# Kernel optimization log

Hardware: AMD Instinct MI355X
Metric: run time of the kernel (lower is better)

## Reference

```python
import jax, jax.numpy as jnp
import numpy as np

T, B, C, H, W = 128, 16, 4, 84, 84
NUM_ACTIONS, FEAT, HID = 18, 512, 256


def _conv(x, w, b, stride):
    # x: (N,C,H,W), w: (O,I,kh,kw)
    y = jax.lax.conv_general_dilated(
        x, w, window_strides=(stride, stride), padding='VALID',
        dimension_numbers=('NCHW', 'OIHW', 'NCHW'))
    return y + b[None, :, None, None]


def setup_inputs() -> dict:
    key = jax.random.key(0)
    ks = jax.random.split(key, 24)
    s = 0.05
    inp = {
        'obs_seq': jax.random.uniform(ks[0], (T, B, C, H, W), jnp.float32) * 255.0,
        'actions_seq': jax.random.randint(ks[1], (T, B), 0, NUM_ACTIONS),
        'episode_starts_seq': jax.random.randint(ks[2], (T, B), 0, 2).astype(jnp.float32),
        'h0': jnp.zeros((1, B, HID), jnp.float32),
        'c0': jnp.zeros((1, B, HID), jnp.float32),
        # NatureCNN params
        'conv1_w': jax.random.normal(ks[3], (32, C, 8, 8)) * s,
        'conv1_b': jnp.zeros((32,)),
        'conv2_w': jax.random.normal(ks[4], (64, 32, 4, 4)) * s,
        'conv2_b': jnp.zeros((64,)),
        'conv3_w': jax.random.normal(ks[5], (64, 64, 3, 3)) * s,
        'conv3_b': jnp.zeros((64,)),
        'fc_w': jax.random.normal(ks[6], (FEAT, 64 * 7 * 7)) * s,
        'fc_b': jnp.zeros((FEAT,)),
        # LSTM params (torch gate order i,f,g,o)
        'w_ih': jax.random.normal(ks[7], (4 * HID, FEAT)) * s,
        'w_hh': jax.random.normal(ks[8], (4 * HID, HID)) * s,
        'b_ih': jnp.zeros((4 * HID,)),
        'b_hh': jnp.zeros((4 * HID,)),
        # heads
        'actor_w': jax.random.normal(ks[9], (NUM_ACTIONS, HID)) * 0.01,
        'actor_b': jnp.zeros((NUM_ACTIONS,)),
        'critic_w': jax.random.normal(ks[10], (1, HID)) * s,
        'critic_b': jnp.zeros((1,)),
        'aux_w': jax.random.normal(ks[11], (1, FEAT)) * s,
        'aux_b': jnp.zeros((1,)),
    }
    return inp


def reference(obs_seq, actions_seq, episode_starts_seq, h0, c0,
              conv1_w, conv1_b, conv2_w, conv2_b, conv3_w, conv3_b,
              fc_w, fc_b, w_ih, w_hh, b_ih, b_hh,
              actor_w, actor_b, critic_w, critic_b, aux_w, aux_b):
    t, b = actions_seq.shape
    x = obs_seq.reshape(t * b, *obs_seq.shape[2:]) / 255.0
    x = jax.nn.relu(_conv(x, conv1_w, conv1_b, 4))   # (TB,32,20,20)
    x = jax.nn.relu(_conv(x, conv2_w, conv2_b, 2))   # (TB,64,9,9)
    x = jax.nn.relu(_conv(x, conv3_w, conv3_b, 1))   # (TB,64,7,7)
    feat = jax.nn.relu(x.reshape(t * b, -1) @ fc_w.T + fc_b)  # (TB,FEAT)

    aux_logits = (feat @ aux_w.T + aux_b).squeeze(-1).reshape(t, b)
    feat_seq = feat.reshape(t, b, -1)

    def step(carry, inp):
        h, c = carry
        x_t, s_t = inp
        keep = (1.0 - s_t)[:, None]
        h = h * keep
        c = c * keep
        gates = x_t @ w_ih.T + b_ih + h @ w_hh.T + b_hh  # (B,4H)
        i, f, g, o = jnp.split(gates, 4, axis=-1)
        c = jax.nn.sigmoid(f) * c + jax.nn.sigmoid(i) * jnp.tanh(g)
        h = jax.nn.sigmoid(o) * jnp.tanh(c)
        return (h, c), h

    _, out = jax.lax.scan(step, (h0[0], c0[0]), (feat_seq, episode_starts_seq))  # (T,B,HID)

    logits = out @ actor_w.T + actor_b
    logp = jax.nn.log_softmax(logits, axis=-1)
    log_probs = jnp.take_along_axis(logp, actions_seq[..., None], axis=-1).squeeze(-1)
    entropy = -jnp.sum(jnp.exp(logp) * logp, axis=-1)
    values = (out @ critic_w.T + critic_b).squeeze(-1)
    return log_probs, entropy, values, aux_logits
```

## Files before the change

### kernel.cpp

```cpp
#include <hip/hip_runtime.h>
#include <hip/hip_bf16.h>
#include <cstddef>

typedef __attribute__((ext_vector_type(8))) short bf16x8;
typedef __attribute__((ext_vector_type(8))) unsigned short u16x8;
typedef __attribute__((ext_vector_type(4))) float f32x4;

static constexpr size_t OFF_X1B   = 0;
static constexpr size_t OFF_X2B   = 52428800;
static constexpr size_t OFF_X3B   = 73662464;
static constexpr size_t OFF_FEATB = 86507520;
static constexpr size_t OFF_W2B   = 88604672;
static constexpr size_t OFF_W3B   = 88670208;
static constexpr size_t OFF_FCWB  = 88743936;
static constexpr size_t OFF_WIHB  = 91955200;
static constexpr size_t OFF_GX    = 97198080;
static constexpr size_t OFF_HSEQ  = 105586688;
static constexpr size_t OFF_W1B   = 108732416;
static constexpr size_t OFF_WHHB  = 108748800;
static constexpr size_t OFF_ORDB  = 109273088;
static constexpr size_t OFF_ORDT0 = 109281280;
static constexpr size_t OFF_ORDLEN= 109289472;
static constexpr size_t OFF_NSEG  = 109297664;
static constexpr size_t OFF_FCPART= 109305856;

__device__ __forceinline__ float sigmoidf_(float x) {
  return 1.0f / (1.0f + __expf(-x));
}
__device__ __forceinline__ float tanhf_(float x) {
  return 1.0f - 2.0f / (__expf(2.0f * x) + 1.0f);
}
__device__ __forceinline__ short f2bfs(float x) {
  union { __hip_bfloat16 b; short s; } cv;
  cv.b = __float2bfloat16(x);
  return cv.s;
}

__global__ __launch_bounds__(256) void prep_kernel(
    const float* __restrict__ c1w, const float* __restrict__ c2w,
    const float* __restrict__ c3w, const float* __restrict__ fcw,
    const float* __restrict__ wih, const float* __restrict__ whh,
    __hip_bfloat16* __restrict__ w1b,
    __hip_bfloat16* __restrict__ w2b, __hip_bfloat16* __restrict__ w3b,
    __hip_bfloat16* __restrict__ fcwb, __hip_bfloat16* __restrict__ wihb,
    __hip_bfloat16* __restrict__ whhb) {
  int i = blockIdx.x * 256 + threadIdx.x;
  if (i < 32768) {
    int o = i >> 9, k = i & 511;
    int pos = k >> 5, ci = k & 31;
    int ky = pos >> 2, kx = pos & 3;
    w2b[i] = __float2bfloat16(c2w[o * 512 + ci * 16 + ky * 4 + kx]);
  } else if (i < 69632) {
    int j = i - 32768;
    int o = j / 576, k = j - o * 576;
    int pos = k >> 6, ci = k & 63;
    int ky = pos / 3, kx = pos - ky * 3;
    w3b[j] = __float2bfloat16(c3w[o * 576 + ci * 9 + ky * 3 + kx]);
  } else if (i < 1675264) {
    int j = i - 69632;
    int o = j / 3136, k = j - o * 3136;
    int sp = k >> 6, ci = k & 63;
    fcwb[j] = __float2bfloat16(fcw[o * 3136 + ci * 49 + sp]);
  } else if (i < 2199552) {
    int j = i - 1675264;
    wihb[j] = __float2bfloat16(wih[j]);
  } else if (i < 2461696) {
    int j = i - 2199552;
    whhb[j] = __float2bfloat16(whh[j]);
  } else if (i < 2469888) {
    int j = i - 2461696;
    int oc = j >> 8, k = j & 255;
    int ky = k >> 5, rem = k & 31;
    int ci = rem >> 3, kx = rem & 7;
    w1b[j] = __float2bfloat16(c1w[oc * 256 + ci * 64 + ky * 8 + kx] * (1.0f / 255.0f));
  }
}

__global__ __launch_bounds__(256) void plan_kernel(
    const float* __restrict__ starts, int* __restrict__ ord_b,
    int* __restrict__ ord_t0, int* __restrict__ ord_len,
    int* __restrict__ nseg_out) {
  __shared__ float s_starts[2048];
  __shared__ int s_t0[2048];
  __shared__ int s_len[2048];
  __shared__ int cnt[16];
  __shared__ int hist[132];
  __shared__ int off[132];
  const int tid = threadIdx.x;
  {
    float4* d = (float4*)s_starts;
    const float4* s = (const float4*)starts;
#pragma unroll
    for (int i = 0; i < 2; ++i) d[tid + i * 256] = s[tid + i * 256];
  }
  if (tid < 132) hist[tid] = 0;
  __syncthreads();
  if (tid < 16) {
    int b = tid, c = 0;
    for (int t = 0; t < 128; ++t) {
      float s = s_starts[t * 16 + b];
      if (t == 0 || s != 0.0f) {
        if (c > 0) s_len[b * 128 + c - 1] = t - s_t0[b * 128 + c - 1];
        s_t0[b * 128 + c] = t;
        ++c;
      }
    }
    s_len[b * 128 + c - 1] = 128 - s_t0[b * 128 + c - 1];
    cnt[b] = c;
  }
  __syncthreads();
  for (int idx = tid; idx < 2048; idx += 256) {
    int b = idx >> 7, i = idx & 127;
    if (i < cnt[b]) atomicAdd(&hist[s_len[idx]], 1);
  }
  __syncthreads();
  if (tid == 0) {
    int running = 0;
    for (int L = 128; L >= 1; --L) { off[L] = running; running += hist[L]; }
    *nseg_out = running;
  }
  __syncthreads();
  for (int idx = tid; idx < 2048; idx += 256) {
    int b = idx >> 7, i = idx & 127;
    if (i < cnt[b]) {
      int len = s_len[idx];
      int pos = atomicAdd(&off[len], 1);
      ord_b[pos] = b;
      ord_t0[pos] = s_t0[idx];
      ord_len[pos] = len;
    }
  }
}

__global__ __launch_bounds__(256, 2) void conv1_rs(
    const float* __restrict__ obs, const __hip_bfloat16* __restrict__ w1b,
    const float* __restrict__ b1, __hip_bfloat16* __restrict__ x1b) {
  constexpr int LDW = 264;
  __shared__ __align__(16) __hip_bfloat16 Ws[32 * LDW];
  const int tid = threadIdx.x;
  const int wv = tid >> 6, l = tid & 63;
  const int lane16 = l & 15, quad = l >> 4;
  for (int i = tid; i < 1024; i += 256) {
    const int r = i >> 5, c = (i & 31) * 8;
    *(uint4*)&Ws[r * LDW + c] = *(const uint4*)&w1b[r * 256 + c];
  }
  const int m0 = blockIdx.x * 256 + wv * 64;
  const float* abase[4];
#pragma unroll
  for (int mf = 0; mf < 4; ++mf) {
    const int m = m0 + mf * 16 + lane16;
    const int n = m / 400, sp = m - n * 400;
    const int oy = sp / 20, ox = sp - oy * 20;
    abase[mf] = obs + (size_t)n * 28224 + quad * 7056 + (oy * 4) * 84 + ox * 4;
  }
  f32x4 acc[4][2] = {};
  __syncthreads();
#pragma unroll 2
  for (int s = 0; s < 8; ++s) {
    bf16x8 bfr[2];
#pragma unroll
    for (int nf = 0; nf < 2; ++nf)
      bfr[nf] = *(const bf16x8*)&Ws[(nf * 16 + lane16) * LDW + s * 32 + quad * 8];
#pragma unroll
    for (int mf = 0; mf < 4; ++mf) {
      const float4 p = *(const float4*)(abase[mf] + s * 84);
      const float4 q = *(const float4*)(abase[mf] + s * 84 + 4);
      bf16x8 a;
      a[0] = f2bfs(p.x); a[1] = f2bfs(p.y); a[2] = f2bfs(p.z); a[3] = f2bfs(p.w);
      a[4] = f2bfs(q.x); a[5] = f2bfs(q.y); a[6] = f2bfs(q.z); a[7] = f2bfs(q.w);
      acc[mf][0] = __builtin_amdgcn_mfma_f32_16x16x32_bf16(a, bfr[0], acc[mf][0], 0, 0, 0);
      acc[mf][1] = __builtin_amdgcn_mfma_f32_16x16x32_bf16(a, bfr[1], acc[mf][1], 0, 0, 0);
    }
  }
#pragma unroll
  for (int nf = 0; nf < 2; ++nf) {
    const int col = nf * 16 + lane16;
    const float bb = b1[col];
#pragma unroll
    for (int mf = 0; mf < 4; ++mf)
#pragma unroll
      for (int r = 0; r < 4; ++r) {
        const int row = m0 + mf * 16 + quad * 4 + r;
        x1b[(size_t)row * 32 + col] =
            __float2bfloat16(fmaxf(acc[mf][nf][r] + bb, 0.f));
      }
  }
}

template<int KK, int LDW, int MODE>
__global__ __launch_bounds__(256, 2) void conv_rs(
    const __hip_bfloat16* __restrict__ A, const __hip_bfloat16* __restrict__ Wb,
    const float* __restrict__ bias, __hip_bfloat16* __restrict__ Cb) {
  __shared__ __align__(16) __hip_bfloat16 Ws[64 * LDW];
  const int tid = threadIdx.x;
  const int wv = tid >> 6, l = tid & 63;
  const int lane16 = l & 15, quad = l >> 4;
  constexpr int CPR = KK / 8;
  constexpr int CH = 64 * CPR;
  for (int i = tid; i < CH; i += 256) {
    const int r = i / CPR;
    const int c = (i - r * CPR) * 8;
    *(uint4*)&Ws[r * LDW + c] = *(const uint4*)&Wb[r * KK + c];
  }
  const int m0 = blockIdx.x * 256 + wv * 64;
  const __hip_bfloat16* abase[4];
#pragma unroll
  for (int mf = 0; mf < 4; ++mf) {
    const int m = m0 + mf * 16 + lane16;
    if (MODE == 1) {
      const int n = m / 81, sp = m - n * 81;
      const int oy = sp / 9, ox = sp - oy * 9;
      abase[mf] = A + ((n * 20 + oy * 2) * 20 + ox * 2) * 32 + quad * 8;
    } else {
      const int n = m / 49, sp = m - n * 49;
      const int oy = sp / 7, ox = sp - oy * 7;
      abase[mf] = A + ((n * 9 + oy) * 9 + ox) * 64 + quad * 8;
    }
  }
  f32x4 acc[4][4] = {};
  __syncthreads();
  constexpr int KS = KK / 32;
#pragma unroll
  for (int s = 0; s < KS; ++s) {
    int koff;
    if (MODE == 1) {
      koff = ((s >> 2) * 20 + (s & 3)) * 32;
    } else {
      const int pos = s >> 1;
      koff = ((pos / 3) * 9 + (pos % 3)) * 64 + (s & 1) * 32;
    }
    bf16x8 bfr[4];
#pragma unroll
    for (int nf = 0; nf < 4; ++nf)
      bfr[nf] = *(const bf16x8*)&Ws[(nf * 16 + lane16) * LDW + s * 32 + quad * 8];
#pragma unroll
    for (int mf = 0; mf < 4; ++mf) {
      const bf16x8 a = *(const bf16x8*)(abase[mf] + koff);
#pragma unroll
      for (int nf = 0; nf < 4; ++nf)
        acc[mf][nf] = __builtin_amdgcn_mfma_f32_16x16x32_bf16(a, bfr[nf], acc[mf][nf], 0, 0, 0);
    }
  }
#pragma unroll
  for (int nf = 0; nf < 4; ++nf) {
    const int col = nf * 16 + lane16;
    const float bb = bias[col];
#pragma unroll
    for (int mf = 0; mf < 4; ++mf)
#pragma unroll
      for (int r = 0; r < 4; ++r) {
        const int row = m0 + mf * 16 + quad * 4 + r;
        Cb[(size_t)row * 64 + col] =
            __float2bfloat16(fmaxf(acc[mf][nf][r] + bb, 0.f));
      }
  }
}

template<int BM, int MODE>
__global__ __launch_bounds__(256) void gemm_mfma(
    const __hip_bfloat16* __restrict__ Abase,
    const __hip_bfloat16* __restrict__ Wb,
    const float* __restrict__ bias1, const float* __restrict__ bias2,
    float* __restrict__ Cf, __hip_bfloat16* __restrict__ Cb,
    const int M, const int N, const int K, const int relu,
    float* __restrict__ Cpart) {
  constexpr int LDK = 40;
  __shared__ __align__(16) __hip_bfloat16 As[BM * LDK];
  __shared__ __align__(16) __hip_bfloat16 Ws[64 * LDK];
  const int tid = threadIdx.x;
  const int m0 = blockIdx.y * BM;
  const int n0 = blockIdx.x * 64;
  const int l = tid & 63;
  const int wv = tid >> 6;
  const int lane16 = l & 15;
  const int quad = l >> 4;
  constexpr int NF = (BM == 128) ? 4 : 2;
  const int m_base = (BM == 128) ? wv * 32 : (wv & 1) * 32;
  const int n_base = (BM == 128) ? 0 : (wv >> 1) * 32;
  constexpr int NCA = (BM == 128) ? 2 : 1;

  f32x4 acc[2][NF] = {};

  const __hip_bfloat16* arow[NCA];
  int acp[NCA];
#pragma unroll
  for (int c = 0; c < NCA; ++c) {
    const int id = tid + c * 256;
    const int row = id >> 2, cpos = id & 3;
    const int m = m0 + row;
    acp[c] = cpos;
    arow[c] = Abase + (size_t)m * K + cpos * 8;
  }
  const int wrow = tid >> 2, wcp = tid & 3;
  const __hip_bfloat16* wsrc = Wb + (size_t)(n0 + wrow) * K + wcp * 8;

  int s0 = 0, s1 = K >> 5;
  if (Cpart) {
    const int total = K >> 5;
    const int zz = blockIdx.z;
    const int q = total >> 2, rr = total & 3;
    s0 = zz * q + (zz < rr ? zz : rr);
    s1 = s0 + q + (zz < rr ? 1 : 0);
  }
  for (int s = s0; s < s1; ++s) {
    uint4 av[NCA];
#pragma unroll
    for (int c = 0; c < NCA; ++c) {
      av[c] = *(const uint4*)(arow[c] + s * 32);
    }
    const uint4 wval = *(const uint4*)(wsrc + s * 32);
    __syncthreads();
#pragma unroll
    for (int c = 0; c < NCA; ++c) {
      const int row = (tid + c * 256) >> 2;
      *(uint4*)&As[row * LDK + acp[c] * 8] = av[c];
    }
    *(uint4*)&Ws[wrow * LDK + wcp * 8] = wval;
    __syncthreads();
    const bf16x8 a0 = *(const bf16x8*)&As[(m_base + lane16) * LDK + quad * 8];
    const bf16x8 a1 = *(const bf16x8*)&As[(m_base + 16 + lane16) * LDK + quad * 8];
#pragma unroll
    for (int nf = 0; nf < NF; ++nf) {
      const bf16x8 b = *(const bf16x8*)&Ws[(n_base + nf * 16 + lane16) * LDK + quad * 8];
      acc[0][nf] = __builtin_amdgcn_mfma_f32_16x16x32_bf16(a0, b, acc[0][nf], 0, 0, 0);
      acc[1][nf] = __builtin_amdgcn_mfma_f32_16x16x32_bf16(a1, b, acc[1][nf], 0, 0, 0);
    }
  }
  if (Cpart) {
    float* dst = Cpart + (size_t)blockIdx.z * M * N;
#pragma unroll
    for (int nf = 0; nf < NF; ++nf) {
      const int col = n0 + n_base + nf * 16 + lane16;
#pragma unroll
      for (int mf = 0; mf < 2; ++mf) {
#pragma unroll
        for (int r = 0; r < 4; ++r) {
          const int row = m0 + m_base + mf * 16 + quad * 4 + r;
          dst[(size_t)row * N + col] = acc[mf][nf][r];
        }
      }
    }
    return;
  }
#pragma unroll
  for (int nf = 0; nf < NF; ++nf) {
    const int col = n0 + n_base + nf * 16 + lane16;
    float bb = bias1[col];
    if (bias2) bb += bias2[col];
#pragma unroll
    for (int mf = 0; mf < 2; ++mf) {
#pragma unroll
      for (int r = 0; r < 4; ++r) {
        const int row = m0 + m_base + mf * 16 + quad * 4 + r;
        float v = acc[mf][nf][r] + bb;
        if (relu) v = fmaxf(v, 0.f);
        if (Cf) Cf[(size_t)row * N + col] = v;
        if (Cb) Cb[(size_t)row * N + col] = __float2bfloat16(v);
      }
    }
  }
}

__global__ __launch_bounds__(256) void fc_reduce(
    const float* __restrict__ part, const float* __restrict__ fcb,
    const float* __restrict__ aux_w, const float* __restrict__ aux_b,
    __hip_bfloat16* __restrict__ featb, float* __restrict__ outp) {
  const int row = blockIdx.x;
  const int tid = threadIdx.x;
  __shared__ float red[256];
  float auxacc = 0.f;
#pragma unroll
  for (int h = 0; h < 2; ++h) {
    const int c = tid + h * 256;
    const size_t base = (size_t)row * 512 + c;
    float v = part[base] + part[1048576 + base] + part[2097152 + base] +
              part[3145728 + base];
    v += fcb[c];
    v = fmaxf(v, 0.f);
    featb[base] = __float2bfloat16(v);
    auxacc += v * aux_w[c];
  }
  red[tid] = auxacc;
  __syncthreads();
  for (int s = 128; s > 0; s >>= 1) {
    if (tid < s) red[tid] += red[tid + s];
    __syncthreads();
  }
  if (tid == 0) outp[6144 + row] = red[0] + aux_b[0];
}

__global__ __launch_bounds__(1024, 4) void lstm_mfma(
    const float* __restrict__ gx, const __hip_bfloat16* __restrict__ whhb,
    const float* __restrict__ starts, const float* __restrict__ h0,
    const float* __restrict__ c0, const int* __restrict__ ord_b,
    const int* __restrict__ ord_t0, const int* __restrict__ ord_len,
    const int* __restrict__ nseg_p, float* __restrict__ hseq) {
  constexpr int LDH = 264;
  constexpr int PS  = 1028;
  __shared__ __align__(16) __hip_bfloat16 h_lds[16 * LDH];
  __shared__ __align__(16) float pre[16 * PS];
  __shared__ int sg_b[16], sg_t0[16], sg_len[16];
  const int g = blockIdx.x;
  const int nseg = *nseg_p;
  if (g * 16 >= nseg) return;
  const int tid = threadIdx.x;
  const int wv = tid >> 6;
  const int l = tid & 63;
  const int lane16 = l & 15, quad = l >> 4;
  if (tid < 16) {
    const int s = g * 16 + tid;
    sg_b[tid] = (s < nseg) ? ord_b[s] : 0;
    sg_t0[tid] = (s < nseg) ? ord_t0[s] : 0;
    sg_len[tid] = (s < nseg) ? ord_len[s] : 0;
  }
  __syncthreads();
  bf16x8 bfrag[2][8];
#pragma unroll
  for (int nt = 0; nt < 2; ++nt)
#pragma unroll
    for (int ks = 0; ks < 8; ++ks)
      bfrag[nt][ks] = *(const bf16x8*)&whhb[
          (size_t)(wv * 64 + nt * 16 + lane16) * 256 + ks * 32 + quad * 8];
  const __hip_bfloat16* bs2 = &whhb[(size_t)(wv * 64 + 32 + lane16) * 256 + quad * 8];
  const __hip_bfloat16* bs3 = &whhb[(size_t)(wv * 64 + 48 + lane16) * 256 + quad * 8];

  const int m_own = wv;
  const int u = l * 4;
  const int b_own = sg_b[m_own];
  const int t0_own = sg_t0[m_own];
  const int len_own = sg_len[m_own];
  float4 c_reg = make_float4(0.f, 0.f, 0.f, 0.f);
  {
    float4 hv = make_float4(0.f, 0.f, 0.f, 0.f);
    if (len_own > 0 && t0_own == 0) {
      const float keep = 1.0f - starts[b_own];
      const float4 h4 = *(const float4*)&h0[b_own * 256 + u];
      const float4 c4 = *(const float4*)&c0[b_own * 256 + u];
      hv = make_float4(h4.x * keep, h4.y * keep, h4.z * keep, h4.w * keep);
      c_reg = make_float4(c4.x * keep, c4.y * keep, c4.z * keep, c4.w * keep);
    }
    __hip_bfloat16* hd = &h_lds[m_own * LDH + u];
    hd[0] = __float2bfloat16(hv.x); hd[1] = __float2bfloat16(hv.y);
    hd[2] = __float2bfloat16(hv.z); hd[3] = __float2bfloat16(hv.w);
  }
  const int maxlen = sg_len[0];
  for (int tt = 0; tt < maxlen; ++tt) {
    __syncthreads();
    f32x4 acc[4] = {};
#pragma unroll
    for (int ks = 0; ks < 8; ++ks) {
      const bf16x8 b2 = *(const bf16x8*)(bs2 + ks * 32);
      const bf16x8 b3 = *(const bf16x8*)(bs3 + ks * 32);
      const bf16x8 a = *(const bf16x8*)&h_lds[lane16 * LDH + ks * 32 + quad * 8];
      acc[0] = __builtin_amdgcn_mfma_f32_16x16x32_bf16(a, bfrag[0][ks], acc[0], 0, 0, 0);
      acc[1] = __builtin_amdgcn_mfma_f32_16x16x32_bf16(a, bfrag[1][ks], acc[1], 0, 0, 0);
      acc[2] = __builtin_amdgcn_mfma_f32_16x16x32_bf16(a, b2, acc[2], 0, 0, 0);
      acc[3] = __builtin_amdgcn_mfma_f32_16x16x32_bf16(a, b3, acc[3], 0, 0, 0);
    }
#pragma unroll
    for (int nt = 0; nt < 4; ++nt)
#pragma unroll
      for (int r = 0; r < 4; ++r)
        pre[(quad * 4 + r) * PS + wv * 64 + nt * 16 + lane16] = acc[nt][r];
    __syncthreads();
    if (tt < len_own) {
      const int t = t0_own + tt;
      const size_t gbase = (size_t)(t * 16 + b_own) * 1024 + u;
      const float4 g0 = *(const float4*)&gx[gbase];
      const float4 g1 = *(const float4*)&gx[gbase + 256];
      const float4 g2 = *(const float4*)&gx[gbase + 512];
      const float4 g3 = *(const float4*)&gx[gbase + 768];
      const float4 p0 = *(const float4*)&pre[m_own * PS + u];
      const float4 p1 = *(const float4*)&pre[m_own * PS + u + 256];
      const float4 p2 = *(const float4*)&pre[m_own * PS + u + 512];
      const float4 p3 = *(const float4*)&pre[m_own * PS + u + 768];
      const float i0 = sigmoidf_(p0.x + g0.x), i1 = sigmoidf_(p0.y + g0.y),
                  i2 = sigmoidf_(p0.z + g0.z), i3 = sigmoidf_(p0.w + g0.w);
      const float f0 = sigmoidf_(p1.x + g1.x), f1 = sigmoidf_(p1.y + g1.y),
                  f2 = sigmoidf_(p1.z + g1.z), f3 = sigmoidf_(p1.w + g1.w);
      const float q0 = tanhf_(p2.x + g2.x), q1 = tanhf_(p2.y + g2.y),
                  q2 = tanhf_(p2.z + g2.z), q3 = tanhf_(p2.w + g2.w);
      const float o0 = sigmoidf_(p3.x + g3.x), o1 = sigmoidf_(p3.y + g3.y),
                  o2 = sigmoidf_(p3.z + g3.z), o3 = sigmoidf_(p3.w + g3.w);
      c_reg.x = fmaf(f0, c_reg.x, i0 * q0);
      c_reg.y = fmaf(f1, c_reg.y, i1 * q1);
      c_reg.z = fmaf(f2, c_reg.z, i2 * q2);
      c_reg.w = fmaf(f3, c_reg.w, i3 * q3);
      const float4 h4 = make_float4(o0 * tanhf_(c_reg.x), o1 * tanhf_(c_reg.y),
                                    o2 * tanhf_(c_reg.z), o3 * tanhf_(c_reg.w));
      __hip_bfloat16* hd = &h_lds[m_own * LDH + u];
      hd[0] = __float2bfloat16(h4.x); hd[1] = __float2bfloat16(h4.y);
      hd[2] = __float2bfloat16(h4.z); hd[3] = __float2bfloat16(h4.w);
      *(float4*)&hseq[(size_t)(t * 16 + b_own) * 256 + u] = h4;
    }
  }
}

__global__ __launch_bounds__(256) void heads_kernel(
    const float* __restrict__ hseq, const int* __restrict__ actions,
    const float* __restrict__ actor_w, const float* __restrict__ actor_b,
    const float* __restrict__ critic_w, const float* __restrict__ critic_b,
    float* __restrict__ outp) {
  const int tid = threadIdx.x;
  const int wv = tid >> 6, l = tid & 63;
  const int tb = blockIdx.x * 4 + wv;
  const float4 h4 = *(const float4*)&hseq[(size_t)tb * 256 + l * 4];
  float part[19];
#pragma unroll
  for (int o = 0; o < 18; ++o) {
    const float4 w = *(const float4*)&actor_w[o * 256 + l * 4];
    part[o] = h4.x * w.x + h4.y * w.y + h4.z * w.z + h4.w * w.w;
  }
  {
    const float4 w = *(const float4*)&critic_w[l * 4];
    part[18] = h4.x * w.x + h4.y * w.y + h4.z * w.z + h4.w * w.w;
  }
#pragma unroll
  for (int off = 32; off > 0; off >>= 1) {
#pragma unroll
    for (int o = 0; o < 19; ++o) part[o] += __shfl_xor(part[o], off);
  }
  float lg[18];
  float m = -1e30f;
#pragma unroll
  for (int o = 0; o < 18; ++o) {
    lg[o] = part[o] + actor_b[o];
    m = fmaxf(m, lg[o]);
  }
  float se = 0.f;
#pragma unroll
  for (int o = 0; o < 18; ++o) se += __expf(lg[o] - m);
  const float lse = __logf(se);
  float ent = 0.f;
#pragma unroll
  for (int o = 0; o < 18; ++o) {
    const float lp = lg[o] - m - lse;
    ent -= __expf(lp) * lp;
  }
  if (l == 0) {
    const int a = actions[tb];
    outp[tb] = lg[a] - m - lse;
    outp[2048 + tb] = ent;
    outp[4096 + tb] = part[18] + critic_b[0];
  }
}

extern "C" void kernel_launch(void* const* d_in, const int* in_sizes, int n_in,
                              void* d_out, int out_size, void* d_ws, size_t ws_size,
                              hipStream_t stream) {
  const float* obs     = (const float*)d_in[0];
  const int*   actions = (const int*)d_in[1];
  const float* starts  = (const float*)d_in[2];
  const float* h0      = (const float*)d_in[3];
  const float* c0      = (const float*)d_in[4];
  const float* c1w     = (const float*)d_in[5];
  const float* c1b     = (const float*)d_in[6];
  const float* c2w     = (const float*)d_in[7];
  const float* c2b     = (const float*)d_in[8];
  const float* c3w     = (const float*)d_in[9];
  const float* c3b     = (const float*)d_in[10];
  const float* fcw     = (const float*)d_in[11];
  const float* fcb     = (const float*)d_in[12];
  const float* wih     = (const float*)d_in[13];
  const float* whh     = (const float*)d_in[14];
  const float* bih     = (const float*)d_in[15];
  const float* bhh     = (const float*)d_in[16];
  const float* aw      = (const float*)d_in[17];
  const float* ab      = (const float*)d_in[18];
  const float* cw      = (const float*)d_in[19];
  const float* cb      = (const float*)d_in[20];
  const float* auxw    = (const float*)d_in[21];
  const float* auxb    = (const float*)d_in[22];

  char* ws = (char*)d_ws;
  __hip_bfloat16* x1b   = (__hip_bfloat16*)(ws + OFF_X1B);
  __hip_bfloat16* x2b   = (__hip_bfloat16*)(ws + OFF_X2B);
  __hip_bfloat16* x3b   = (__hip_bfloat16*)(ws + OFF_X3B);
  __hip_bfloat16* featb = (__hip_bfloat16*)(ws + OFF_FEATB);
  __hip_bfloat16* w2b   = (__hip_bfloat16*)(ws + OFF_W2B);
  __hip_bfloat16* w3b   = (__hip_bfloat16*)(ws + OFF_W3B);
  __hip_bfloat16* fcwb  = (__hip_bfloat16*)(ws + OFF_FCWB);
  __hip_bfloat16* wihb  = (__hip_bfloat16*)(ws + OFF_WIHB);
  __hip_bfloat16* w1b   = (__hip_bfloat16*)(ws + OFF_W1B);
  __hip_bfloat16* whhb  = (__hip_bfloat16*)(ws + OFF_WHHB);
  float* gx   = (float*)(ws + OFF_GX);
  float* hseq = (float*)(ws + OFF_HSEQ);
  int* ord_b   = (int*)(ws + OFF_ORDB);
  int* ord_t0  = (int*)(ws + OFF_ORDT0);
  int* ord_len = (int*)(ws + OFF_ORDLEN);
  int* nseg    = (int*)(ws + OFF_NSEG);
  float* fcpart= (float*)(ws + OFF_FCPART);
  float* outp = (float*)d_out;

  prep_kernel<<<9648, 256, 0, stream>>>(c1w, c2w, c3w, fcw, wih, whh,
                                        w1b, w2b, w3b, fcwb, wihb, whhb);
  plan_kernel<<<1, 256, 0, stream>>>(starts, ord_b, ord_t0, ord_len, nseg);
  conv1_rs<<<3200, 256, 0, stream>>>(obs, w1b, c1b, x1b);
  conv_rs<512, 520, 1><<<648, 256, 0, stream>>>(x1b, w2b, c2b, x2b);
  conv_rs<576, 584, 2><<<392, 256, 0, stream>>>(x2b, w3b, c3b, x3b);
  gemm_mfma<64, 0><<<dim3(8, 32, 4), 256, 0, stream>>>(
      x3b, fcwb, fcb, nullptr, nullptr, nullptr, 2048, 512, 3136, 0, fcpart);
  fc_reduce<<<2048, 256, 0, stream>>>(fcpart, fcb, auxw, auxb, featb, outp);
  gemm_mfma<64, 0><<<dim3(16, 32), 256, 0, stream>>>(
      featb, wihb, bih, bhh, gx, nullptr, 2048, 1024, 512, 0, nullptr);
  lstm_mfma<<<128, 1024, 0, stream>>>(gx, whhb, starts, h0, c0,
                                      ord_b, ord_t0, ord_len, nseg, hseq);
  heads_kernel<<<512, 256, 0, stream>>>(hseq, actions, aw, ab, cw, cb, outp);
}
```

Baseline: 688.9 us.

## Stage whole observation image in LDS as bf16 for conv1

Conv1 now runs one block per image. The block loads the full 4x84x84 float observation once with coalesced float4 reads, converts it to bf16 and stores it in shared memory with rows interleaved by channel. The im2col A fragments are then read from LDS instead of strided global loads. This removes repeated global reads and repeated float-to-bf16 conversion of overlapping 8x8 windows. In exchange it uses about 56KB of LDS per block, which limits occupancy, and each wave handles fewer output tiles.

```diff
diff --git a/kernel.cpp b/kernel.cpp
--- a/kernel.cpp
+++ b/kernel.cpp
@@ -30,10 +30,10 @@
 __device__ __forceinline__ float tanhf_(float x) {
   return 1.0f - 2.0f / (__expf(2.0f * x) + 1.0f);
 }
-__device__ __forceinline__ short f2bfs(float x) {
-  union { __hip_bfloat16 b; short s; } cv;
+__device__ __forceinline__ unsigned short f2bfu(float x) {
+  union { __hip_bfloat16 b; unsigned short u; } cv;
   cv.b = __float2bfloat16(x);
-  return cv.s;
+  return cv.u;
 }
 
 __global__ __launch_bounds__(256) void prep_kernel(
@@ -132,58 +132,62 @@
   }
 }
 
-__global__ __launch_bounds__(256, 2) void conv1_rs(
+__global__ __launch_bounds__(256, 2) void conv1_img(
     const float* __restrict__ obs, const __hip_bfloat16* __restrict__ w1b,
-    const float* __restrict__ b1, __hip_bfloat16* __restrict__ x1b) {
+    const float* __restrict__ bias1, __hip_bfloat16* __restrict__ x1b) {
   constexpr int LDW = 264;
+  __shared__ __align__(16) __hip_bfloat16 img[28224];
   __shared__ __align__(16) __hip_bfloat16 Ws[32 * LDW];
   const int tid = threadIdx.x;
   const int wv = tid >> 6, l = tid & 63;
   const int lane16 = l & 15, quad = l >> 4;
+  const int n = blockIdx.x;
+
   for (int i = tid; i < 1024; i += 256) {
     const int r = i >> 5, c = (i & 31) * 8;
     *(uint4*)&Ws[r * LDW + c] = *(const uint4*)&w1b[r * 256 + c];
   }
-  const int m0 = blockIdx.x * 256 + wv * 64;
-  const float* abase[4];
-#pragma unroll
-  for (int mf = 0; mf < 4; ++mf) {
-    const int m = m0 + mf * 16 + lane16;
-    const int n = m / 400, sp = m - n * 400;
+  const float4* obs4 = (const float4*)(obs + (size_t)n * 28224);
+  for (int j = tid; j < 7056; j += 256) {
+    const float4 v = obs4[j];
+    const int xq = j % 21;
+    const int yc = j / 21;
+    const int c = yc / 84, y = yc - c * 84;
+    ushort4 w;
+    w.x = f2bfu(v.x); w.y = f2bfu(v.y); w.z = f2bfu(v.z); w.w = f2bfu(v.w);
+    *(ushort4*)&img[(y * 4 + c) * 84 + xq * 4] = w;
+  }
+  __syncthreads();
+
+  const float bb0 = bias1[lane16];
+  const float bb1 = bias1[16 + lane16];
+  const __hip_bfloat16* wr0 = &Ws[lane16 * LDW];
+  const __hip_bfloat16* wr1 = &Ws[(16 + lane16) * LDW];
+
+  for (int f = wv; f < 25; f += 4) {
+    const int sp = f * 16 + lane16;
     const int oy = sp / 20, ox = sp - oy * 20;
-    abase[mf] = obs + (size_t)n * 28224 + quad * 7056 + (oy * 4) * 84 + ox * 4;
-  }
-  f32x4 acc[4][2] = {};
-  __syncthreads();
-#pragma unroll 2
-  for (int s = 0; s < 8; ++s) {
-    bf16x8 bfr[2];
-#pragma unroll
-    for (int nf = 0; nf < 2; ++nf)
-      bfr[nf] = *(const bf16x8*)&Ws[(nf * 16 + lane16) * LDW + s * 32 + quad * 8];
-#pragma unroll
-    for (int mf = 0; mf < 4; ++mf) {
-      const float4 p = *(const float4*)(abase[mf] + s * 84);
-      const float4 q = *(const float4*)(abase[mf] + s * 84 + 4);
+    const int ab = ((oy * 4) * 4 + quad) * 84 + ox * 4;
+    f32x4 acc0 = {}, acc1 = {};
+#pragma unroll
+    for (int s = 0; s < 8; ++s) {
+      const int ib = ab + s * 4 * 84;
+      const ushort4 lo = *(const ushort4*)&img[ib];
+      const ushort4 hi = *(const ushort4*)&img[ib + 4];
       bf16x8 a;
-      a[0] = f2bfs(p.x); a[1] = f2bfs(p.y); a[2] = f2bfs(p.z); a[3] = f2bfs(p.w);
-      a[4] = f2bfs(q.x); a[5] = f2bfs(q.y); a[6] = f2bfs(q.z); a[7] = f2bfs(q.w);
-      acc[mf][0] = __builtin_amdgcn_mfma_f32_16x16x32_bf16(a, bfr[0], acc[mf][0], 0, 0, 0);
-      acc[mf][1] = __builtin_amdgcn_mfma_f32_16x16x32_bf16(a, bfr[1], acc[mf][1], 0, 0, 0);
-    }
-  }
-#pragma unroll
-  for (int nf = 0; nf < 2; ++nf) {
-    const int col = nf * 16 + lane16;
-    const float bb = b1[col];
-#pragma unroll
-    for (int mf = 0; mf < 4; ++mf)
-#pragma unroll
-      for (int r = 0; r < 4; ++r) {
-        const int row = m0 + mf * 16 + quad * 4 + r;
-        x1b[(size_t)row * 32 + col] =
-            __float2bfloat16(fmaxf(acc[mf][nf][r] + bb, 0.f));
-      }
+      a[0] = (short)lo.x; a[1] = (short)lo.y; a[2] = (short)lo.z; a[3] = (short)lo.w;
+      a[4] = (short)hi.x; a[5] = (short)hi.y; a[6] = (short)hi.z; a[7] = (short)hi.w;
+      const bf16x8 b0 = *(const bf16x8*)&wr0[s * 32 + quad * 8];
+      const bf16x8 b1v = *(const bf16x8*)&wr1[s * 32 + quad * 8];
+      acc0 = __builtin_amdgcn_mfma_f32_16x16x32_bf16(a, b0, acc0, 0, 0, 0);
+      acc1 = __builtin_amdgcn_mfma_f32_16x16x32_bf16(a, b1v, acc1, 0, 0, 0);
+    }
+#pragma unroll
+    for (int r = 0; r < 4; ++r) {
+      const size_t row = (size_t)n * 400 + f * 16 + quad * 4 + r;
+      x1b[row * 32 + lane16] = __float2bfloat16(fmaxf(acc0[r] + bb0, 0.f));
+      x1b[row * 32 + 16 + lane16] = __float2bfloat16(fmaxf(acc1[r] + bb1, 0.f));
+    }
   }
 }
 
@@ -595,7 +599,7 @@
   prep_kernel<<<9648, 256, 0, stream>>>(c1w, c2w, c3w, fcw, wih, whh,
                                         w1b, w2b, w3b, fcwb, wihb, whhb);
   plan_kernel<<<1, 256, 0, stream>>>(starts, ord_b, ord_t0, ord_len, nseg);
-  conv1_rs<<<3200, 256, 0, stream>>>(obs, w1b, c1b, x1b);
+  conv1_img<<<2048, 256, 0, stream>>>(obs, w1b, c1b, x1b);
   conv_rs<512, 520, 1><<<648, 256, 0, stream>>>(x1b, w2b, c2b, x2b);
   conv_rs<576, 584, 2><<<392, 256, 0, stream>>>(x2b, w3b, c3b, x3b);
   gemm_mfma<64, 0><<<dim3(8, 32, 4), 256, 0, stream>>>(
```

After: 658.3 us. -4.4%, faster.
